# Performance work log

Measured on AMD Instinct MI355X. Metric: run time of the kernel, lower is better.

## Reference

```python
import jax, jax.numpy as jnp
import numpy as np

NUM_CLASS = 80
STRIDES = (8, 16, 32, 64, 128)
IMG = 1024
B = 16
NMS_PRE = 1000        # test_cfg['nms_pre']
SCORE_THR = 0.05      # test_cfg['score_thr']
IOU_THR = 0.5         # test_cfg['iou_threshold']
MAX_PER_IMG = 100     # test_cfg['max_per_img']
NMS_CAND = 2000       # fixed-size candidate set for jit-compatible NMS


def _level_hw():
    return [IMG // s for s in STRIDES]


def setup_inputs() -> dict:
    key = jax.random.key(0)
    inp = {}
    i = 0
    for li, hw in enumerate(_level_hw()):
        inp[f"cls{li}"] = jax.random.normal(jax.random.fold_in(key, i), (B, NUM_CLASS, hw, hw), jnp.float32); i += 1
        inp[f"bbox{li}"] = jax.random.uniform(jax.random.fold_in(key, i), (B, 4, hw, hw), jnp.float32) * 64.0; i += 1
        inp[f"ctr{li}"] = jax.random.normal(jax.random.fold_in(key, i), (B, 1, hw, hw), jnp.float32); i += 1
    inp["image_sizes"] = jnp.full((B, 2), IMG, jnp.int32)  # (h, w) per image
    return inp


def _mesh(hw, stride):
    # generate_single_meshgrids: grid of point centers, (hw*hw, 2) as (x, y)
    r = jnp.arange(hw, dtype=jnp.float32) * stride + stride // 2
    yy, xx = jnp.meshgrid(r, r, indexing="ij")
    return jnp.stack([xx.reshape(-1), yy.reshape(-1)], axis=-1)


def _decode(dist, mesh, max_xy):
    # distance2bbox with max_shape clamping
    b = jnp.stack([mesh[..., 0] - dist[..., 0], mesh[..., 1] - dist[..., 1],
                   mesh[..., 0] + dist[..., 2], mesh[..., 1] + dist[..., 3]], axis=-1)
    return jnp.clip(b, 0.0, max_xy)


def _iou(box, bxs):
    lt = jnp.maximum(box[:2], bxs[:, :2])
    rb = jnp.minimum(box[2:], bxs[:, 2:])
    wh = jnp.clip(rb - lt, 0.0, None)
    inter = wh[:, 0] * wh[:, 1]
    a1 = (box[2] - box[0]) * (box[3] - box[1])
    a2 = (bxs[:, 2] - bxs[:, 0]) * (bxs[:, 3] - bxs[:, 1])
    return inter / jnp.maximum(a1 + a2 - inter, 1e-6)


def _single_image(cls_l, bbox_l, ctr_l, meshes, max_xy):
    sc_all, bx_all, ct_all = [], [], []
    for cls, bbox, ctr, mesh in zip(cls_l, bbox_l, ctr_l, meshes):
        n = mesh.shape[0]
        scores = jax.nn.sigmoid(cls.reshape(NUM_CLASS, n).T)   # (n, C)
        dist = bbox.reshape(4, n).T                             # (n, 4)
        ctrn = jax.nn.sigmoid(ctr.reshape(n))                   # (n,)
        k = min(NMS_PRE, n)
        _, idx = jax.lax.top_k(scores.max(axis=1), k)           # nms_pre pre-filter
        sc_all.append(scores[idx])
        bx_all.append(_decode(dist[idx], mesh[idx], max_xy))
        ct_all.append(ctrn[idx])
    scores = jnp.concatenate(sc_all)   # (N, C)
    boxes = jnp.concatenate(bx_all)    # (N, 4)
    ctrn = jnp.concatenate(ct_all)     # (N,)
    final = scores * ctrn[:, None]
    final = jnp.where(final > SCORE_THR, final, 0.0)  # score_thr filter (masked)
    top_s, top_i = jax.lax.top_k(final.reshape(-1), NMS_CAND)
    box_i = top_i // NUM_CLASS
    labels = top_i % NUM_CLASS
    bxs = boxes[box_i]
    # class-offset trick for class-aware NMS
    off = bxs + labels[:, None].astype(bxs.dtype) * (IMG + 1.0)

    def step(s, _):
        j = jnp.argmax(s)
        valid = s[j] > 0.0
        ob = jnp.where(valid, bxs[j], 0.0)
        osc = jnp.where(valid, s[j], 0.0)
        ol = jnp.where(valid, labels[j], -1)
        s_new = jnp.where(_iou(off[j], off) >= IOU_THR, 0.0, s)
        return s_new, (ob, osc, ol)

    _, (kb, ks, kl) = jax.lax.scan(step, top_s, None, length=MAX_PER_IMG)
    dets = jnp.concatenate([kb, ks[:, None]], axis=-1)  # (max_per_img, 5)
    return dets, kl


def reference(cls0, bbox0, ctr0, cls1, bbox1, ctr1, cls2, bbox2, ctr2,
              cls3, bbox3, ctr3, cls4, bbox4, ctr4, image_sizes):
    meshes = [_mesh(hw, s) for hw, s in zip(_level_hw(), STRIDES)]
    hw = image_sizes.astype(jnp.float32)  # (B, 2) = (h, w)
    max_xy = jnp.stack([hw[:, 1], hw[:, 0], hw[:, 1], hw[:, 0]], axis=-1)  # (B, 4)
    cls_l = (cls0, cls1, cls2, cls3, cls4)
    bbox_l = (bbox0, bbox1, bbox2, bbox3, bbox4)
    ctr_l = (ctr0, ctr1, ctr2, ctr3, ctr4)
    f = lambda c, b, t, m: _single_image(c, b, t, meshes, m)
    dets, labels = jax.vmap(f)(cls_l, bbox_l, ctr_l, max_xy)
    return dets, labels
```

## Files before the change

kernel.cpp:

```cpp
#include <hip/hip_runtime.h>
#include <cstdint>
#include <cstddef>

#define NCLS   80
#define NB     16
#define NPTS   21824
#define NSEL   3320
#define NTOT   (NSEL*NCLS)
#define NCAND  2000
#define MAXPER 100
#define TCHUNK 66400
#define TIECAP 4096
#define TIECAP_SEL 4096

__device__ __forceinline__ float sigmoidf_(float x){ return 1.0f/(1.0f+expf(-x)); }
__device__ __forceinline__ unsigned fkey(float f){
    unsigned u = __float_as_uint(f);
    return (u & 0x80000000u) ? ~u : (u | 0x80000000u);
}

__device__ __forceinline__ void wave_hist_add(unsigned* hist, int bucket, bool active){
    unsigned long long rem = __ballot(active);
    int lane = threadIdx.x & 63;
    while (rem){
        int leader = __ffsll((long long)rem) - 1;
        int lb = __shfl(bucket, leader);
        unsigned long long match = __ballot(active && bucket == lb);
        if (lane == leader) atomicAdd(&hist[lb], (unsigned)__popcll(match));
        rem &= ~match;
    }
}

__global__ void k_maxscore(const float* __restrict__ c0, const float* __restrict__ c1,
                           const float* __restrict__ c2, const float* __restrict__ c3,
                           const float* __restrict__ c4, float* __restrict__ maxscore){
    const int GP = NPTS/4;
    int g = blockIdx.x*blockDim.x + threadIdx.x;
    if (g >= NB*GP) return;
    int b = g / GP, r = (g - b*GP)*4;
    const float* cls; int n, p;
    if      (r < 16384){ cls=c0; n=16384; p=r; }
    else if (r < 20480){ cls=c1; n=4096;  p=r-16384; }
    else if (r < 21504){ cls=c2; n=1024;  p=r-20480; }
    else if (r < 21760){ cls=c3; n=256;   p=r-21504; }
    else               { cls=c4; n=64;    p=r-21760; }
    const float* base = cls + (size_t)b*NCLS*n + p;
    float4 m = make_float4(-3.4e38f,-3.4e38f,-3.4e38f,-3.4e38f);
    #pragma unroll 8
    for (int c = 0; c < NCLS; ++c){
        const float4 v = *(const float4*)(base + (size_t)c*n);
        m.x = fmaxf(m.x, v.x); m.y = fmaxf(m.y, v.y);
        m.z = fmaxf(m.z, v.z); m.w = fmaxf(m.w, v.w);
    }
    float4 s = make_float4(sigmoidf_(m.x), sigmoidf_(m.y), sigmoidf_(m.z), sigmoidf_(m.w));
    *(float4*)(maxscore + (size_t)b*NPTS + r) = s;
}

__global__ void __launch_bounds__(1024) k_select(const float* __restrict__ maxscore,
                                                 int* __restrict__ sel){
    int blk = blockIdx.x; int b = blk/5, li = blk - 5*b;
    int n, k, poff, soff;
    if      (li==0){ n=16384; k=1000; poff=0;     soff=0;    }
    else if (li==1){ n=4096;  k=1000; poff=16384; soff=1000; }
    else if (li==2){ n=1024;  k=1000; poff=20480; soff=2000; }
    else if (li==3){ n=256;   k=256;  poff=21504; soff=3000; }
    else           { n=64;    k=64;   poff=21760; soff=3256; }
    const float* x = maxscore + b*NPTS + poff;
    int* out = sel + b*NSEL + soff;
    int tid = threadIdx.x, nt = blockDim.x;
    if (k == n){ for (int i=tid;i<n;i+=nt) out[i]=i; return; }

    __shared__ unsigned suf[256];
    __shared__ int sh_d, sh_s1, s_cnt, s_tc;
    __shared__ float tk[TIECAP_SEL];
    __shared__ int   ti[TIECAP_SEL];

    for (int i=tid;i<256;i+=nt) suf[i]=0u;
    if (tid==0){ s_cnt=0; s_tc=0; }
    __syncthreads();
    for (int i0=0;i0<n;i0+=nt){
        int i=i0+tid; bool act=(i<n);
        int bkt = act ? (int)(fkey(x[i])>>24) : 0;
        wave_hist_add(suf, bkt, act);
    }
    __syncthreads();
    for (int o=1;o<256;o<<=1){
        unsigned v=(tid<256 && tid+o<256)?suf[tid+o]:0u; __syncthreads();
        if (tid<256) suf[tid]+=v; __syncthreads();
    }
    if (tid<256){
        unsigned s1=(tid<255)?suf[tid+1]:0u;
        if (suf[tid]>=(unsigned)k && s1<(unsigned)k){ sh_d=tid; sh_s1=(int)s1; }
    }
    __syncthreads();
    int T8 = sh_d, base8 = sh_s1, r8 = k - sh_s1;
    __syncthreads();
    for (int i=tid;i<256;i+=nt) suf[i]=0u;
    __syncthreads();
    for (int i0=0;i0<n;i0+=nt){
        int i=i0+tid; bool act=false; int bkt=0;
        if (i<n){ unsigned key=fkey(x[i]); act=((int)(key>>24)==T8); bkt=(int)((key>>16)&255u); }
        wave_hist_add(suf, bkt, act);
    }
    __syncthreads();
    for (int o=1;o<256;o<<=1){
        unsigned v=(tid<256 && tid+o<256)?suf[tid+o]:0u; __syncthreads();
        if (tid<256) suf[tid]+=v; __syncthreads();
    }
    if (tid<256){
        unsigned s1=(tid<255)?suf[tid+1]:0u;
        if (suf[tid]>=(unsigned)r8 && s1<(unsigned)r8){ sh_d=tid; sh_s1=(int)s1; }
    }
    __syncthreads();
    int T16 = (T8<<8) | sh_d;
    int base = base8 + sh_s1;
    int r = r8 - sh_s1;
    for (int i=tid;i<n;i+=nt){
        int k16 = (int)(fkey(x[i])>>16);
        if (k16 > T16) out[atomicAdd(&s_cnt,1)] = i;
        else if (k16 == T16){
            int p = atomicAdd(&s_tc,1);
            if (p < TIECAP_SEL){ tk[p]=x[i]; ti[p]=i; }
        }
    }
    __syncthreads();
    int m = s_tc; if (m > TIECAP_SEL) m = TIECAP_SEL;
    for (int i=tid;i<m;i+=nt){
        unsigned ki = fkey(tk[i]); int ii = ti[i]; int rk = 0;
        for (int j=0;j<m;++j){
            unsigned kj = fkey(tk[j]);
            rk += (kj>ki || (kj==ki && ti[j]<ii)) ? 1 : 0;
        }
        if (rk < r) out[base+rk] = ii;
    }
}

__global__ void k_gather(const float* __restrict__ c0, const float* __restrict__ c1,
                         const float* __restrict__ c2, const float* __restrict__ c3,
                         const float* __restrict__ c4,
                         const float* __restrict__ b0, const float* __restrict__ b1,
                         const float* __restrict__ b2, const float* __restrict__ b3,
                         const float* __restrict__ b4,
                         const float* __restrict__ t0, const float* __restrict__ t1,
                         const float* __restrict__ t2, const float* __restrict__ t3,
                         const float* __restrict__ t4,
                         const int* __restrict__ imsz, const int* __restrict__ sel,
                         float* __restrict__ boxes, float* __restrict__ finals){
    size_t i = (size_t)blockIdx.x*blockDim.x + threadIdx.x;
    const size_t total = (size_t)NB*NTOT;
    if (i >= total) return;
    int b = (int)(i / NTOT);
    int r = (int)(i - (size_t)b*NTOT);
    int slot = r / NCLS, c = r - slot*NCLS;
    const float *cls, *bb, *ct; int n, hw, st;
    if      (slot < 1000){ cls=c0; bb=b0; ct=t0; n=16384; hw=128; st=8;   }
    else if (slot < 2000){ cls=c1; bb=b1; ct=t1; n=4096;  hw=64;  st=16;  }
    else if (slot < 3000){ cls=c2; bb=b2; ct=t2; n=1024;  hw=32;  st=32;  }
    else if (slot < 3256){ cls=c3; bb=b3; ct=t3; n=256;   hw=16;  st=64;  }
    else                 { cls=c4; bb=b4; ct=t4; n=64;    hw=8;   st=128; }
    int p = sel[b*NSEL + slot];
    float ctrn = sigmoidf_(ct[(size_t)b*n + p]);
    float sc = sigmoidf_(cls[((size_t)b*NCLS + c)*n + p]) * ctrn;
    finals[(size_t)b*NTOT + r] = (sc > 0.05f) ? sc : 0.0f;
    if (c == 0){
        const float* base = bb + (size_t)b*4*n;
        float d0 = base[p], d1 = base[n+p], d2 = base[2*n+p], d3 = base[3*n+p];
        int py = p / hw, px = p - py*hw;
        float mx = (float)(px*st + st/2), my = (float)(py*st + st/2);
        float w = (float)imsz[b*2+1], h = (float)imsz[b*2+0];
        float x1 = fminf(fmaxf(mx - d0, 0.0f), w);
        float y1 = fminf(fmaxf(my - d1, 0.0f), h);
        float x2 = fminf(fmaxf(mx + d2, 0.0f), w);
        float y2 = fminf(fmaxf(my + d3, 0.0f), h);
        float* bo = boxes + ((size_t)b*NSEL + slot)*4;
        bo[0]=x1; bo[1]=y1; bo[2]=x2; bo[3]=y2;
    }
}

__global__ void k_zero(unsigned* __restrict__ ghA){
    int i = blockIdx.x*blockDim.x + threadIdx.x;
    if (i < NB*256) ghA[i] = 0u;
}

__global__ void __launch_bounds__(1024) k_topA(const float* __restrict__ finals,
                                               unsigned* __restrict__ ghA){
    int img = blockIdx.x >> 2, part = blockIdx.x & 3;
    const float* x = finals + (size_t)img*NTOT;
    __shared__ unsigned h[256];
    int tid = threadIdx.x, nt = blockDim.x;
    for (int i=tid;i<256;i+=nt) h[i]=0u;
    __syncthreads();
    int lo = part*TCHUNK, hi = lo + TCHUNK;
    for (int i0=lo;i0<hi;i0+=nt){
        int i = i0 + tid; bool act = (i < hi);
        int bkt = act ? (int)(fkey(x[i])>>24) : 0;
        wave_hist_add(h, bkt, act);
    }
    __syncthreads();
    for (int i=tid;i<256;i+=nt) if (h[i]) atomicAdd(&ghA[img*256+i], h[i]);
}

__global__ void k_threshA(const unsigned* __restrict__ ghA, unsigned* __restrict__ ghB,
                          int* __restrict__ prm){
    int img = blockIdx.x, tid = threadIdx.x;
    __shared__ unsigned suf[256];
    suf[tid] = ghA[img*256+tid];
    ghB[img*256+tid] = 0u;
    __syncthreads();
    for (int o=1;o<256;o<<=1){
        unsigned v = (tid+o<256)?suf[tid+o]:0u; __syncthreads();
        suf[tid]+=v; __syncthreads();
    }
    unsigned s1 = (tid<255)?suf[tid+1]:0u;
    if (suf[tid] >= (unsigned)NCAND && s1 < (unsigned)NCAND){
        prm[img*8+0]=tid; prm[img*8+1]=NCAND-(int)s1; prm[img*8+2]=(int)s1;
    }
}

__global__ void __launch_bounds__(1024) k_topB(const float* __restrict__ finals,
                                               const int* __restrict__ prm,
                                               unsigned* __restrict__ ghB){
    int img = blockIdx.x >> 2, part = blockIdx.x & 3;
    const float* x = finals + (size_t)img*NTOT;
    int T8 = prm[img*8+0];
    __shared__ unsigned h[256];
    int tid = threadIdx.x, nt = blockDim.x;
    for (int i=tid;i<256;i+=nt) h[i]=0u;
    __syncthreads();
    int lo = part*TCHUNK, hi = lo + TCHUNK;
    for (int i0=lo;i0<hi;i0+=nt){
        int i = i0 + tid; bool act=false; int bkt=0;
        if (i < hi){ unsigned key=fkey(x[i]); act=((int)(key>>24)==T8); bkt=(int)((key>>16)&255u); }
        wave_hist_add(h, bkt, act);
    }
    __syncthreads();
    for (int i=tid;i<256;i+=nt) if (h[i]) atomicAdd(&ghB[img*256+i], h[i]);
}

__global__ void k_threshB(const unsigned* __restrict__ ghB, int* __restrict__ prm){
    int img = blockIdx.x, tid = threadIdx.x;
    __shared__ unsigned suf[256];
    int T8 = prm[img*8+0], r8 = prm[img*8+1], base8 = prm[img*8+2];
    suf[tid] = ghB[img*256+tid];
    __syncthreads();
    for (int o=1;o<256;o<<=1){
        unsigned v = (tid+o<256)?suf[tid+o]:0u; __syncthreads();
        suf[tid]+=v; __syncthreads();
    }
    unsigned s1 = (tid<255)?suf[tid+1]:0u;
    if (suf[tid] >= (unsigned)r8 && s1 < (unsigned)r8){
        prm[img*8+3]=(T8<<8)|tid;
        prm[img*8+4]=base8+(int)s1;
        prm[img*8+5]=r8-(int)s1;
    }
    if (tid==0){ prm[img*8+6]=0; prm[img*8+7]=0; }
}

__global__ void __launch_bounds__(1024) k_compact(const float* __restrict__ finals,
                                                  const float* __restrict__ boxes,
                                                  int* __restrict__ prm,
                                                  float* __restrict__ cscore,
                                                  float* __restrict__ cbox,
                                                  int* __restrict__ clab,
                                                  float* __restrict__ tieS,
                                                  int* __restrict__ tieI){
    int img = blockIdx.x >> 2, part = blockIdx.x & 3;
    const float* x = finals + (size_t)img*NTOT;
    int T16 = prm[img*8+3];
    int* appc = &prm[img*8+6];
    int* tiec = &prm[img*8+7];
    int tid = threadIdx.x, nt = blockDim.x, lane = tid & 63;
    int lo = part*TCHUNK, hi = lo + TCHUNK;
    for (int i0=lo;i0<hi;i0+=nt){
        int i = i0 + tid;
        bool insel=false, intie=false;
        if (i < hi){
            int k16 = (int)(fkey(x[i])>>16);
            insel = (k16 > T16); intie = (k16 == T16);
        }
        unsigned long long mk = __ballot(insel);
        if (mk){
            int ldr = __ffsll((long long)mk)-1; int pb=0;
            if (lane==ldr) pb = atomicAdd(appc, __popcll(mk));
            pb = __shfl(pb, ldr);
            if (insel){
                int pos = pb + __popcll(mk & ((1ull<<lane)-1ull));
                int ci = img*NCAND + pos;
                int slot = i/NCLS, lab = i - slot*NCLS;
                cscore[ci] = x[i]; clab[ci] = lab;
                *(float4*)(cbox + (size_t)ci*4) = *(const float4*)(boxes + ((size_t)img*NSEL + slot)*4);
            }
        }
        unsigned long long mt = __ballot(intie);
        if (mt){
            int ldr = __ffsll((long long)mt)-1; int pb=0;
            if (lane==ldr) pb = atomicAdd(tiec, __popcll(mt));
            pb = __shfl(pb, ldr);
            if (intie){
                int p = pb + __popcll(mt & ((1ull<<lane)-1ull));
                if (p < TIECAP){ tieS[img*TIECAP+p] = x[i]; tieI[img*TIECAP+p] = i; }
            }
        }
    }
}

__global__ void __launch_bounds__(1024) k_ties(const int* __restrict__ prm,
                                               const float* __restrict__ tieS,
                                               const int* __restrict__ tieI,
                                               const float* __restrict__ boxes,
                                               float* __restrict__ cscore,
                                               float* __restrict__ cbox,
                                               int* __restrict__ clab){
    int img = blockIdx.x, tid = threadIdx.x, nt = blockDim.x;
    int base = prm[img*8+4], r = prm[img*8+5];
    int m = prm[img*8+7]; if (m > TIECAP) m = TIECAP;
    __shared__ float sk[TIECAP];
    __shared__ int   si[TIECAP];
    for (int i=tid;i<m;i+=nt){ sk[i]=tieS[img*TIECAP+i]; si[i]=tieI[img*TIECAP+i]; }
    __syncthreads();
    for (int i=tid;i<m;i+=nt){
        unsigned ki = fkey(sk[i]); int ii = si[i]; int rk = 0;
        for (int j=0;j<m;++j){
            unsigned kj = fkey(sk[j]);
            rk += (kj>ki || (kj==ki && si[j]<ii)) ? 1 : 0;
        }
        if (rk < r){
            int ci = img*NCAND + base + rk;
            int slot = ii/NCLS, lab = ii - slot*NCLS;
            cscore[ci] = sk[i]; clab[ci] = lab;
            *(float4*)(cbox + (size_t)ci*4) = *(const float4*)(boxes + ((size_t)img*NSEL + slot)*4);
        }
    }
}

__global__ void __launch_bounds__(256) k_nms(const float* __restrict__ cscore,
                                             const float* __restrict__ cbox,
                                             const int*   __restrict__ clab,
                                             float* __restrict__ out){
    int b = blockIdx.x, tid = threadIdx.x;
    float s[8], x0[8], y0[8], x1[8], y1[8];
    __shared__ float lcbox[2048][4];
    __shared__ int   llab[2048];
    __shared__ float rv[4]; __shared__ int ri[4];
    __shared__ float sbx[4];
    #pragma unroll
    for (int k=0;k<8;++k){
        int i = k*256 + tid;
        if (i < NCAND){
            int ci = b*NCAND + i;
            float4 bb = *(const float4*)(cbox + (size_t)ci*4);
            int lab = clab[ci];
            float sc = cscore[ci];
            lcbox[i][0]=bb.x; lcbox[i][1]=bb.y; lcbox[i][2]=bb.z; lcbox[i][3]=bb.w;
            llab[i] = lab;
            float lo = 1025.0f * (float)lab;
            s[k]=sc; x0[k]=bb.x+lo; y0[k]=bb.y+lo; x1[k]=bb.z+lo; y1[k]=bb.w+lo;
        } else {
            lcbox[i][0]=0; lcbox[i][1]=0; lcbox[i][2]=0; lcbox[i][3]=0;
            llab[i]=0;
            s[k]=0.0f; x0[k]=0; y0[k]=0; x1[k]=0; y1[k]=0;
        }
    }
    __syncthreads();
    for (int it = 0; it < MAXPER; ++it){
        float v = s[0]; int bi = tid;
        #pragma unroll
        for (int k=1;k<8;++k){ if (s[k] > v){ v = s[k]; bi = k*256 + tid; } }
        #pragma unroll
        for (int off=32; off>=1; off>>=1){
            float ov = __shfl_xor(v, off);
            int   oi = __shfl_xor(bi, off);
            if (ov > v || (ov == v && oi < bi)){ v = ov; bi = oi; }
        }
        if ((tid & 63) == 0){ rv[tid>>6] = v; ri[tid>>6] = bi; }
        __syncthreads();
        float vj = rv[0]; int j = ri[0];
        #pragma unroll
        for (int w=1; w<4; ++w){
            if (rv[w] > vj || (rv[w] == vj && ri[w] < j)){ vj = rv[w]; j = ri[w]; }
        }
        if (tid == (j & 255)){
            int k = j >> 8;
            sbx[0]=x0[k]; sbx[1]=y0[k]; sbx[2]=x1[k]; sbx[3]=y1[k];
        }
        if (tid == 0){
            bool valid = vj > 0.0f;
            float* det = out + ((size_t)b*MAXPER + it)*5;
            det[0] = valid ? lcbox[j][0] : 0.0f;
            det[1] = valid ? lcbox[j][1] : 0.0f;
            det[2] = valid ? lcbox[j][2] : 0.0f;
            det[3] = valid ? lcbox[j][3] : 0.0f;
            det[4] = valid ? vj : 0.0f;
            out[NB*MAXPER*5 + b*MAXPER + it] = valid ? (float)llab[j] : -1.0f;
        }
        __syncthreads();
        float jx0=sbx[0], jy0=sbx[1], jx1=sbx[2], jy1=sbx[3];
        float a1 = (jx1-jx0)*(jy1-jy0);
        #pragma unroll
        for (int k=0;k<8;++k){
            float lt0 = fmaxf(jx0, x0[k]), lt1 = fmaxf(jy0, y0[k]);
            float rb0 = fminf(jx1, x1[k]), rb1 = fminf(jy1, y1[k]);
            float w = fmaxf(rb0-lt0, 0.0f), h = fmaxf(rb1-lt1, 0.0f);
            float inter = w*h;
            float a2 = (x1[k]-x0[k])*(y1[k]-y0[k]);
            float iou = inter / fmaxf(a1 + a2 - inter, 1e-6f);
            if (iou >= 0.5f) s[k] = 0.0f;
        }
    }
}

extern "C" void kernel_launch(void* const* d_in, const int* in_sizes, int n_in,
                              void* d_out, int out_size, void* d_ws, size_t ws_size,
                              hipStream_t stream){
    const float *c[5], *bx[5], *ct[5];
    for (int l=0;l<5;++l){
        c[l]  = (const float*)d_in[3*l+0];
        bx[l] = (const float*)d_in[3*l+1];
        ct[l] = (const float*)d_in[3*l+2];
    }
    const int* imsz = (const int*)d_in[15];
    float* ws        = (float*)d_ws;
    float*    maxscore = ws;
    int*      sel      = (int*)(ws + 349184);
    float*    boxes    = ws + 402304;
    float*    finals   = ws + 614784;
    float*    cscore   = ws + 4864384;
    float*    cbox     = ws + 4896384;
    int*      clab     = (int*)(ws + 5024384);
    unsigned* ghA      = (unsigned*)(ws + 5056384);
    unsigned* ghB      = (unsigned*)(ws + 5060480);
    int*      prm      = (int*)(ws + 5064576);
    float*    tieS     = ws + 5064704;
    int*      tieI     = (int*)(ws + 5130240);
    float* out = (float*)d_out;

    k_zero<<<dim3(16), dim3(256), 0, stream>>>(ghA);
    k_maxscore<<<dim3((NB*(NPTS/4) + 255)/256), dim3(256), 0, stream>>>(
        c[0],c[1],c[2],c[3],c[4], maxscore);
    k_select<<<dim3(NB*5), dim3(1024), 0, stream>>>(maxscore, sel);
    size_t total = (size_t)NB*NTOT;
    k_gather<<<dim3((unsigned)((total + 255)/256)), dim3(256), 0, stream>>>(
        c[0],c[1],c[2],c[3],c[4],
        bx[0],bx[1],bx[2],bx[3],bx[4],
        ct[0],ct[1],ct[2],ct[3],ct[4],
        imsz, sel, boxes, finals);
    k_topA<<<dim3(NB*4), dim3(1024), 0, stream>>>(finals, ghA);
    k_threshA<<<dim3(NB), dim3(256), 0, stream>>>(ghA, ghB, prm);
    k_topB<<<dim3(NB*4), dim3(1024), 0, stream>>>(finals, prm, ghB);
    k_threshB<<<dim3(NB), dim3(256), 0, stream>>>(ghB, prm);
    k_compact<<<dim3(NB*4), dim3(1024), 0, stream>>>(finals, boxes, prm, cscore, cbox, clab, tieS, tieI);
    k_ties<<<dim3(NB), dim3(1024), 0, stream>>>(prm, tieS, tieI, boxes, cscore, cbox, clab);
    k_nms<<<dim3(NB), dim3(256), 0, stream>>>(cscore, cbox, clab, out);
}
```

Baseline: 607.4 us.

## Cut NMS loop to one barrier per iteration via packed atomicMax argmax

After: 589.5 us. -3.0%, faster.

```diff
diff --git a/kernel.cpp b/kernel.cpp
--- a/kernel.cpp
+++ b/kernel.cpp
@@ -338,11 +338,11 @@
                                              const int*   __restrict__ clab,
                                              float* __restrict__ out){
     int b = blockIdx.x, tid = threadIdx.x;
-    float s[8], x0[8], y0[8], x1[8], y1[8];
+    float s[8], x0[8], y0[8], x1[8], y1[8], a2[8];
+    __shared__ float obx[2048][4];
     __shared__ float lcbox[2048][4];
     __shared__ int   llab[2048];
-    __shared__ float rv[4]; __shared__ int ri[4];
-    __shared__ float sbx[4];
+    __shared__ unsigned long long pslot[3];
     #pragma unroll
     for (int k=0;k<8;++k){
         int i = k*256 + tid;
@@ -350,18 +350,24 @@
             int ci = b*NCAND + i;
             float4 bb = *(const float4*)(cbox + (size_t)ci*4);
             int lab = clab[ci];
-            float sc = cscore[ci];
+            s[k] = cscore[ci];
             lcbox[i][0]=bb.x; lcbox[i][1]=bb.y; lcbox[i][2]=bb.z; lcbox[i][3]=bb.w;
             llab[i] = lab;
             float lo = 1025.0f * (float)lab;
-            s[k]=sc; x0[k]=bb.x+lo; y0[k]=bb.y+lo; x1[k]=bb.z+lo; y1[k]=bb.w+lo;
+            float ox0=bb.x+lo, oy0=bb.y+lo, ox1=bb.z+lo, oy1=bb.w+lo;
+            obx[i][0]=ox0; obx[i][1]=oy0; obx[i][2]=ox1; obx[i][3]=oy1;
+            x0[k]=ox0; y0[k]=oy0; x1[k]=ox1; y1[k]=oy1;
+            a2[k]=(ox1-ox0)*(oy1-oy0);
         } else {
+            s[k]=0.0f; x0[k]=0.0f; y0[k]=0.0f; x1[k]=0.0f; y1[k]=0.0f; a2[k]=0.0f;
+            obx[i][0]=0; obx[i][1]=0; obx[i][2]=0; obx[i][3]=0;
             lcbox[i][0]=0; lcbox[i][1]=0; lcbox[i][2]=0; lcbox[i][3]=0;
             llab[i]=0;
-            s[k]=0.0f; x0[k]=0; y0[k]=0; x1[k]=0; y1[k]=0;
-        }
-    }
-    __syncthreads();
+        }
+    }
+    if (tid < 3) pslot[tid] = 0ull;
+    __syncthreads();
+    int p = 0;
     for (int it = 0; it < MAXPER; ++it){
         float v = s[0]; int bi = tid;
         #pragma unroll
@@ -372,17 +378,13 @@
             int   oi = __shfl_xor(bi, off);
             if (ov > v || (ov == v && oi < bi)){ v = ov; bi = oi; }
         }
-        if ((tid & 63) == 0){ rv[tid>>6] = v; ri[tid>>6] = bi; }
+        if ((tid & 63) == 0)
+            atomicMax(&pslot[p], ((unsigned long long)fkey(v) << 32) | (unsigned)~bi);
         __syncthreads();
-        float vj = rv[0]; int j = ri[0];
-        #pragma unroll
-        for (int w=1; w<4; ++w){
-            if (rv[w] > vj || (rv[w] == vj && ri[w] < j)){ vj = rv[w]; j = ri[w]; }
-        }
-        if (tid == (j & 255)){
-            int k = j >> 8;
-            sbx[0]=x0[k]; sbx[1]=y0[k]; sbx[2]=x1[k]; sbx[3]=y1[k];
-        }
+        unsigned long long pk = pslot[p];
+        int j = (int)(~(unsigned)pk);
+        float vj = __uint_as_float(((unsigned)(pk >> 32)) & 0x7FFFFFFFu);
+        float jx0 = obx[j][0], jy0 = obx[j][1], jx1 = obx[j][2], jy1 = obx[j][3];
         if (tid == 0){
             bool valid = vj > 0.0f;
             float* det = out + ((size_t)b*MAXPER + it)*5;
@@ -392,9 +394,9 @@
             det[3] = valid ? lcbox[j][3] : 0.0f;
             det[4] = valid ? vj : 0.0f;
             out[NB*MAXPER*5 + b*MAXPER + it] = valid ? (float)llab[j] : -1.0f;
-        }
-        __syncthreads();
-        float jx0=sbx[0], jy0=sbx[1], jx1=sbx[2], jy1=sbx[3];
+            int q = p + 2; if (q >= 3) q -= 3;
+            pslot[q] = 0ull;
+        }
         float a1 = (jx1-jx0)*(jy1-jy0);
         #pragma unroll
         for (int k=0;k<8;++k){
@@ -402,10 +404,10 @@
             float rb0 = fminf(jx1, x1[k]), rb1 = fminf(jy1, y1[k]);
             float w = fmaxf(rb0-lt0, 0.0f), h = fmaxf(rb1-lt1, 0.0f);
             float inter = w*h;
-            float a2 = (x1[k]-x0[k])*(y1[k]-y0[k]);
-            float iou = inter / fmaxf(a1 + a2 - inter, 1e-6f);
+            float iou = inter / fmaxf(a1 + a2[k] - inter, 1e-6f);
             if (iou >= 0.5f) s[k] = 0.0f;
         }
+        ++p; if (p == 3) p = 0;
     }
 }
 
```
